# Performance work log

Hardware: AMD Instinct MI355X
Metric: run time of the kernel (lower is better)

Reference implementation:

```python
import jax, jax.numpy as jnp
import numpy as np

S_D, I_D, O_D = 256, 64, 64
BATCH, T = 64, 2048


def setup_inputs() -> dict:
    key = jax.random.key(0)
    ks = jax.random.split(key, 9)
    # state/inputs and raw standard-normal noise draws (torch.randn equivalents)
    state = jax.random.normal(ks[0], (BATCH, S_D), dtype=jnp.float32)
    inputs = jax.random.normal(ks[1], (BATCH, T, I_D), dtype=jnp.float32)
    eps_W = jax.random.normal(ks[2], (BATCH, T, S_D), dtype=jnp.float32)
    eps_V = jax.random.normal(ks[3], (BATCH, T, O_D), dtype=jnp.float32)
    # system matrices; F scaled to spectral radius ~0.95 (stable system)
    F = jax.random.normal(ks[4], (S_D, S_D), dtype=jnp.float32) * (0.95 / np.sqrt(S_D))
    B_mat = jax.random.normal(ks[5], (S_D, I_D), dtype=jnp.float32)
    H = jax.random.normal(ks[6], (O_D, S_D), dtype=jnp.float32)
    SNR = 2.0
    sqrt_S_W = jax.random.normal(ks[7], (S_D, S_D), dtype=jnp.float32) / SNR
    sqrt_S_V = jax.random.normal(ks[8], (O_D, O_D), dtype=jnp.float32) / SNR
    return {"state": state, "inputs": inputs, "eps_W": eps_W, "eps_V": eps_V,
            "F": F, "B_mat": B_mat, "H": H, "sqrt_S_W": sqrt_S_W, "sqrt_S_V": sqrt_S_V}


def reference(state, inputs, eps_W, eps_V, F, B_mat, H, sqrt_S_W, sqrt_S_V):
    # per-step drive: u_t = inputs_t @ B^T + W_t, with W_t = eps_W_t @ sqrt_S_W^T
    U = jnp.einsum('bti,si->bts', inputs, B_mat) + jnp.einsum('bts,ds->btd', eps_W, sqrt_S_W)
    V = jnp.einsum('bto,po->btp', eps_V, sqrt_S_V)  # [B, T, O_D]

    def step(s, u_t):  # s: [B, S_D], u_t: [B, S_D]
        s = s @ F.T + u_t
        return s, s

    _, states_t = jax.lax.scan(step, state, jnp.swapaxes(U, 0, 1))  # [T, B, S_D]
    states = jnp.swapaxes(states_t, 0, 1)  # [B, T, S_D]
    observations = jnp.einsum('bts,os->bto', states, H) + V  # [B, T, O_D]
    return states, observations
```

## Files before the change

kernel.cpp:

```cpp
#include <hip/hip_runtime.h>
#include <hip/hip_bf16.h>

#define S_DIM 256
#define I_DIM 64
#define O_DIM 64
#define BATCH 64
#define TT 2048
#define CHUNK 32
#define NCHUNK (TT / CHUNK)
#define NTASK (BATCH * TT / CHUNK)

typedef __attribute__((ext_vector_type(8))) short short8v;
typedef _Float16 half8v __attribute__((ext_vector_type(8)));
typedef __attribute__((ext_vector_type(4))) float float4v;

__device__ inline unsigned short f2bf(float f) {
  unsigned x = __float_as_uint(f);
  unsigned r = (x + 0x7FFFu + ((x >> 16) & 1u)) >> 16;
  return (unsigned short)r;
}
__device__ inline short bfr(float x) {
  __hip_bfloat16 h = __float2bfloat16(x);
  return __builtin_bit_cast(short, h);
}

__device__ inline void gload16(const float* g, float* lds) {
  __builtin_amdgcn_global_load_lds(
      (const __attribute__((address_space(1))) unsigned int*)g,
      (__attribute__((address_space(3))) unsigned int*)lds, 16, 0, 0);
}

__global__ void k_matsq(const float* __restrict__ src, float* __restrict__ dst) {
  const int i = blockIdx.x;
  const int j = threadIdx.x;
  float acc = 0.f;
#pragma unroll 8
  for (int k = 0; k < 256; ++k) acc += src[i * 256 + k] * src[k * 256 + j];
  dst[i * 256 + j] = acc;
}

__global__ void k_fsplit16(const float* __restrict__ src, _Float16* __restrict__ hi,
                           _Float16* __restrict__ lo) {
  int idx = blockIdx.x * 256 + threadIdx.x;
  float a = src[idx];
  _Float16 h = (_Float16)a;
  hi[idx] = h;
  lo[idx] = (_Float16)(a - (float)h);
}

__global__ void k_wcvt(const float* __restrict__ s1, const float* __restrict__ s2,
                       int K1, int K2, unsigned short* __restrict__ hi, int total) {
  int idx = blockIdx.x * 256 + threadIdx.x;
  if (idx >= total) return;
  int KT = K1 + K2;
  int n = idx / KT, k = idx - n * KT;
  float a = (k < K1) ? s1[n * K1 + k] : s2[n * K2 + (k - K1)];
  hi[idx] = f2bf(a);
}

template <int N_TOT, int K1, int K2, int M_TILE, int WIM, int WIN>
__global__ __launch_bounds__(256, 3) void k_tgemm(
    const float* __restrict__ A1, const float* __restrict__ A2,
    const unsigned short* __restrict__ W, float* __restrict__ out) {
  constexpr int KT = K1 + K2;
  constexpr int NKT = KT / 64;
  constexpr int MF = M_TILE / WIM / 16;
  constexpr int NF = N_TOT / WIN / 16;
  constexpr int LOGM = (M_TILE == 64) ? 6 : 7;
  constexpr int CPW = M_TILE / 16;

  __shared__ float als[2][M_TILE * 64];

  const int tid = threadIdx.x;
  const int wv = tid >> 6, lane = tid & 63;
  const int lo16 = lane & 15, hi4 = lane >> 4;
  const int wm = wv % WIM, wn = wv / WIM;
  const size_t R0 = (size_t)blockIdx.x * M_TILE;
  const int C0 = wn * (N_TOT / WIN);

  auto stage = [&](int buf, int kt) {
#pragma unroll
    for (int c = 0; c < CPW; ++c) {
      const int i = wv * CPW + c;
      const int s = i * 64 + lane;
      const int row = s & (M_TILE - 1);
      const int g = s >> LOGM;
      const int k0 = kt * 64;
      const float* src = (k0 < K1) ? A1 + (R0 + row) * K1 + k0 + g * 4
                                   : A2 + (R0 + row) * K2 + (k0 - K1) + g * 4;
      gload16(src, &als[buf][i * 256]);
    }
  };
  auto aread = [&](int buf, int kkl, int m, int h) -> float4 {
    const int row = wm * (M_TILE / WIM) + m * 16 + lo16;
    const int g = kkl * 8 + hi4 * 2 + h;
    return *reinterpret_cast<const float4*>(&als[buf][(g * M_TILE + row) * 4]);
  };
  auto wload = [&](int kk, int nf) -> short8v {
    return *reinterpret_cast<const short8v*>(
        W + (size_t)(C0 + nf * 16 + lo16) * KT + kk * 32 + hi4 * 8);
  };

  float4v acc[MF][NF];
#pragma unroll
  for (int m = 0; m < MF; ++m)
#pragma unroll
    for (int n = 0; n < NF; ++n) acc[m][n] = (float4v){0.f, 0.f, 0.f, 0.f};

  short8v wr[2][NF];
  stage(0, 0);
#pragma unroll
  for (int nf = 0; nf < NF; ++nf) wr[0][nf] = wload(0, nf);
  __syncthreads();

#pragma unroll
  for (int kt = 0; kt < NKT; ++kt) {
    if (kt + 1 < NKT) stage((kt + 1) & 1, kt + 1);
#pragma unroll
    for (int kkl = 0; kkl < 2; ++kkl) {
      const int kk = kt * 2 + kkl;
      if (kk + 1 < 2 * NKT) {
#pragma unroll
        for (int nf = 0; nf < NF; ++nf) wr[(kk + 1) & 1][nf] = wload(kk + 1, nf);
      }
      short8v ah[MF];
#pragma unroll
      for (int m = 0; m < MF; ++m) {
        float4 f0 = aread(kt & 1, kkl, m, 0);
        float4 f1 = aread(kt & 1, kkl, m, 1);
#pragma unroll
        for (int j = 0; j < 4; ++j) {
          ah[m][j] = bfr((&f0.x)[j]);
          ah[m][j + 4] = bfr((&f1.x)[j]);
        }
      }
#pragma unroll
      for (int nf = 0; nf < NF; ++nf)
#pragma unroll
        for (int m = 0; m < MF; ++m)
          acc[m][nf] = __builtin_amdgcn_mfma_f32_16x16x32_bf16(
              ah[m], wr[kk & 1][nf], acc[m][nf], 0, 0, 0);
    }
    __syncthreads();
  }

#pragma unroll
  for (int m = 0; m < MF; ++m)
#pragma unroll
    for (int nf = 0; nf < NF; ++nf) {
      const size_t r_base = R0 + wm * (M_TILE / WIM) + m * 16 + hi4 * 4;
      const int col = C0 + nf * 16 + lo16;
#pragma unroll
      for (int rr = 0; rr < 4; ++rr)
        out[(r_base + rr) * N_TOT + col] = acc[m][nf][rr];
    }
}

template <int MODE>
__global__ __launch_bounds__(1024, 4) void k_mscan(const _Float16* __restrict__ Fhi,
                                                   const _Float16* __restrict__ Flo,
                                                   float* __restrict__ U,
                                                   const float* __restrict__ E,
                                                   float* __restrict__ Lst) {
  __shared__ _Float16 sh[16 * 264];
  __shared__ _Float16 sl[16 * 264];

  const int tid = threadIdx.x;
  const int wv = tid >> 6;
  const int l = tid & 63;
  const int lo16 = l & 15, hi4 = l >> 4;
  const int dcol = wv * 16 + lo16;

  const int c = blockIdx.x >> 2;
  const int b0 = (blockIdx.x & 3) * 16;

  half8v fh[8], fl[8];
#pragma unroll
  for (int kk = 0; kk < 8; ++kk) {
    const size_t fo = (size_t)dcol * 256 + kk * 32 + hi4 * 8;
    fh[kk] = *reinterpret_cast<const half8v*>(Fhi + fo);
    fl[kk] = *reinterpret_cast<const half8v*>(Flo + fo);
  }

  if (MODE == 1) {
#pragma unroll
    for (int r = 0; r < 4; ++r) {
      const int m = hi4 * 4 + r;
      float x = E[((size_t)c * BATCH + b0 + m) * 256 + dcol];
      _Float16 h = (_Float16)x;
      sh[m * 264 + dcol] = h;
      sl[m * 264 + dcol] = (_Float16)(x - (float)h);
    }
    __syncthreads();
  }

  const size_t ustr = (size_t)TT * 256;
  float* ub = U + ((size_t)b0 * TT + c * CHUNK) * 256 + dcol;

  float u_cur[4], u_nxt[4];
#pragma unroll
  for (int r = 0; r < 4; ++r) u_cur[r] = ub[(size_t)(hi4 * 4 + r) * ustr];

  for (int k = 0; k < CHUNK; ++k) {
    if (k < CHUNK - 1) {
#pragma unroll
      for (int r = 0; r < 4; ++r)
        u_nxt[r] = ub[(size_t)(hi4 * 4 + r) * ustr + (k + 1) * 256];
    }
    float4v a0, a1, a2;
#pragma unroll
    for (int r = 0; r < 4; ++r) {
      a0[r] = u_cur[r];
      a1[r] = 0.f;
      a2[r] = 0.f;
    }

    if (MODE == 1 || k) {
#pragma unroll
      for (int kk = 0; kk < 8; ++kk) {
        const int ao = lo16 * 264 + kk * 32 + hi4 * 8;
        half8v ah = *reinterpret_cast<const half8v*>(&sh[ao]);
        half8v al = *reinterpret_cast<const half8v*>(&sl[ao]);
        a0 = __builtin_amdgcn_mfma_f32_16x16x32_f16(ah, fh[kk], a0, 0, 0, 0);
        a1 = __builtin_amdgcn_mfma_f32_16x16x32_f16(ah, fl[kk], a1, 0, 0, 0);
        a2 = __builtin_amdgcn_mfma_f32_16x16x32_f16(al, fh[kk], a2, 0, 0, 0);
      }
    }

    _Float16 xh[4], xl[4];
#pragma unroll
    for (int r = 0; r < 4; ++r) {
      float x = a0[r] + a1[r] + a2[r];
      if (MODE == 1) ub[(size_t)(hi4 * 4 + r) * ustr + k * 256] = x;
      if (MODE == 0 && k == CHUNK - 1)
        Lst[((size_t)c * BATCH + b0 + hi4 * 4 + r) * 256 + dcol] = x;
      _Float16 h = (_Float16)x;
      xh[r] = h;
      xl[r] = (_Float16)(x - (float)h);
    }
    __syncthreads();
#pragma unroll
    for (int r = 0; r < 4; ++r) {
      const int m = hi4 * 4 + r;
      sh[m * 264 + dcol] = xh[r];
      sl[m * 264 + dcol] = xl[r];
    }
    __syncthreads();
#pragma unroll
    for (int r = 0; r < 4; ++r) u_cur[r] = u_nxt[r];
  }
}

__global__ __launch_bounds__(1024, 4) void k_mcarry(const _Float16* __restrict__ FLhi,
                                                    const _Float16* __restrict__ FLlo,
                                                    const float* __restrict__ state0,
                                                    const float* __restrict__ Lst,
                                                    float* __restrict__ E) {
  __shared__ _Float16 sh[16 * 264];
  __shared__ _Float16 sl[16 * 264];

  const int tid = threadIdx.x;
  const int wv = tid >> 6;
  const int l = tid & 63;
  const int lo16 = l & 15, hi4 = l >> 4;
  const int dcol = wv * 16 + lo16;
  const int b0 = blockIdx.x * 16;

  half8v fh[8], fl[8];
#pragma unroll
  for (int kk = 0; kk < 8; ++kk) {
    const size_t fo = (size_t)dcol * 256 + kk * 32 + hi4 * 8;
    fh[kk] = *reinterpret_cast<const half8v*>(FLhi + fo);
    fl[kk] = *reinterpret_cast<const half8v*>(FLlo + fo);
  }

#pragma unroll
  for (int r = 0; r < 4; ++r) {
    const int m = hi4 * 4 + r;
    float x = state0[(size_t)(b0 + m) * 256 + dcol];
    E[(size_t)(b0 + m) * 256 + dcol] = x;
    _Float16 h = (_Float16)x;
    sh[m * 264 + dcol] = h;
    sl[m * 264 + dcol] = (_Float16)(x - (float)h);
  }
  __syncthreads();

  for (int cstep = 0; cstep < NCHUNK - 1; ++cstep) {
    float4v a0, a1, a2;
#pragma unroll
    for (int r = 0; r < 4; ++r) {
      a0[r] = Lst[((size_t)cstep * BATCH + b0 + hi4 * 4 + r) * 256 + dcol];
      a1[r] = 0.f;
      a2[r] = 0.f;
    }
#pragma unroll
    for (int kk = 0; kk < 8; ++kk) {
      const int ao = lo16 * 264 + kk * 32 + hi4 * 8;
      half8v ah = *reinterpret_cast<const half8v*>(&sh[ao]);
      half8v al = *reinterpret_cast<const half8v*>(&sl[ao]);
      a0 = __builtin_amdgcn_mfma_f32_16x16x32_f16(ah, fh[kk], a0, 0, 0, 0);
      a1 = __builtin_amdgcn_mfma_f32_16x16x32_f16(ah, fl[kk], a1, 0, 0, 0);
      a2 = __builtin_amdgcn_mfma_f32_16x16x32_f16(al, fh[kk], a2, 0, 0, 0);
    }
    _Float16 xh[4], xl[4];
#pragma unroll
    for (int r = 0; r < 4; ++r) {
      float x = a0[r] + a1[r] + a2[r];
      E[((size_t)(cstep + 1) * BATCH + b0 + hi4 * 4 + r) * 256 + dcol] = x;
      _Float16 h = (_Float16)x;
      xh[r] = h;
      xl[r] = (_Float16)(x - (float)h);
    }
    __syncthreads();
#pragma unroll
    for (int r = 0; r < 4; ++r) {
      const int m = hi4 * 4 + r;
      sh[m * 264 + dcol] = xh[r];
      sl[m * 264 + dcol] = xl[r];
    }
    __syncthreads();
  }
}

extern "C" void kernel_launch(void* const* d_in, const int* in_sizes, int n_in,
                              void* d_out, int out_size, void* d_ws, size_t ws_size,
                              hipStream_t stream) {
  const float* state  = (const float*)d_in[0];
  const float* inputs = (const float*)d_in[1];
  const float* eps_W  = (const float*)d_in[2];
  const float* eps_V  = (const float*)d_in[3];
  const float* F      = (const float*)d_in[4];
  const float* B_mat  = (const float*)d_in[5];
  const float* H      = (const float*)d_in[6];
  const float* SW     = (const float*)d_in[7];
  const float* SV     = (const float*)d_in[8];

  float* out = (float*)d_out;
  float* states_out = out;
  float* obs_out = out + (size_t)BATCH * TT * S_DIM;

  unsigned short* ws16 = (unsigned short*)d_ws;
  unsigned short* whi1 = ws16;
  unsigned short* whi2 = whi1 + 81920;
  _Float16* Fhi  = (_Float16*)(whi2 + 20480);
  _Float16* Flo  = Fhi + 65536;
  _Float16* FLhi = Flo + 65536;
  _Float16* FLlo = FLhi + 65536;

  float* Lst = obs_out;
  float* E   = Lst + (size_t)NCHUNK * BATCH * 256;
  float* Pa  = E + (size_t)NCHUNK * BATCH * 256;
  float* Pb  = Pa + 65536;

  k_matsq<<<256, 256, 0, stream>>>(F, Pa);
  k_matsq<<<256, 256, 0, stream>>>(Pa, Pb);
  k_matsq<<<256, 256, 0, stream>>>(Pb, Pa);
  k_matsq<<<256, 256, 0, stream>>>(Pa, Pb);
  k_matsq<<<256, 256, 0, stream>>>(Pb, Pa);

  k_fsplit16<<<256, 256, 0, stream>>>(F, Fhi, Flo);
  k_fsplit16<<<256, 256, 0, stream>>>(Pa, FLhi, FLlo);

  k_wcvt<<<320, 256, 0, stream>>>(B_mat, SW, 64, 256, whi1, 256 * 320);
  k_wcvt<<<80, 256, 0, stream>>>(H, SV, 256, 64, whi2, 64 * 320);

  k_tgemm<256, 64, 256, 64, 1, 4><<<BATCH * TT / 64, 256, 0, stream>>>(
      inputs, eps_W, whi1, states_out);

  k_mscan<0><<<NTASK / 16, 1024, 0, stream>>>(Fhi, Flo, states_out, E, Lst);

  k_mcarry<<<BATCH / 16, 1024, 0, stream>>>(FLhi, FLlo, state, Lst, E);

  k_mscan<1><<<NTASK / 16, 1024, 0, stream>>>(Fhi, Flo, states_out, E, Lst);

  k_tgemm<64, 256, 64, 128, 4, 1><<<BATCH * TT / 128, 256, 0, stream>>>(
      states_out, eps_V, whi2, obs_out);
}
```

Baseline: 425.0 us.

## Stage full 64x320 activation tile in LDS at once for GEMM kernels

Replaces the double-buffered K-tile streaming GEMM with a kernel that loads the whole 64-row by 320-wide fp32 activation tile into 80 KB of dynamic shared memory up front, then runs all MFMA steps with a single barrier. Weights are loaded directly per step instead of being register double-buffered. The output GEMM also switches from 128-row to 64-row tiles. This removes per-K-tile barriers and staging overlap, but the large LDS footprint limits occupancy to about one block per CU, so global-load latency is no longer hidden behind compute.

```diff
diff --git a/kernel.cpp b/kernel.cpp
--- a/kernel.cpp
+++ b/kernel.cpp
@@ -58,48 +58,39 @@
   hi[idx] = f2bf(a);
 }
 
-template <int N_TOT, int K1, int K2, int M_TILE, int WIM, int WIN>
-__global__ __launch_bounds__(256, 3) void k_tgemm(
-    const float* __restrict__ A1, const float* __restrict__ A2,
+template <int N_TOT, bool SMALL_FIRST, int WIM, int WIN>
+__global__ __launch_bounds__(256) void k_sgemm(
+    const float* __restrict__ Abig, const float* __restrict__ Asmall,
     const unsigned short* __restrict__ W, float* __restrict__ out) {
-  constexpr int KT = K1 + K2;
-  constexpr int NKT = KT / 64;
-  constexpr int MF = M_TILE / WIM / 16;
+  constexpr int KT = 320;
+  constexpr int MF = 64 / WIM / 16;
   constexpr int NF = N_TOT / WIN / 16;
-  constexpr int LOGM = (M_TILE == 64) ? 6 : 7;
-  constexpr int CPW = M_TILE / 16;
-
-  __shared__ float als[2][M_TILE * 64];
+  extern __shared__ float ls[];
 
   const int tid = threadIdx.x;
   const int wv = tid >> 6, lane = tid & 63;
   const int lo16 = lane & 15, hi4 = lane >> 4;
   const int wm = wv % WIM, wn = wv / WIM;
-  const size_t R0 = (size_t)blockIdx.x * M_TILE;
+  const size_t R0 = (size_t)blockIdx.x * 64;
   const int C0 = wn * (N_TOT / WIN);
 
-  auto stage = [&](int buf, int kt) {
-#pragma unroll
-    for (int c = 0; c < CPW; ++c) {
-      const int i = wv * CPW + c;
+#pragma unroll
+  for (int kt = 0; kt < 4; ++kt)
+#pragma unroll
+    for (int c = 0; c < 4; ++c) {
+      const int i = wv * 4 + c;
       const int s = i * 64 + lane;
-      const int row = s & (M_TILE - 1);
-      const int g = s >> LOGM;
-      const int k0 = kt * 64;
-      const float* src = (k0 < K1) ? A1 + (R0 + row) * K1 + k0 + g * 4
-                                   : A2 + (R0 + row) * K2 + (k0 - K1) + g * 4;
-      gload16(src, &als[buf][i * 256]);
-    }
-  };
-  auto aread = [&](int buf, int kkl, int m, int h) -> float4 {
-    const int row = wm * (M_TILE / WIM) + m * 16 + lo16;
-    const int g = kkl * 8 + hi4 * 2 + h;
-    return *reinterpret_cast<const float4*>(&als[buf][(g * M_TILE + row) * 4]);
-  };
-  auto wload = [&](int kk, int nf) -> short8v {
-    return *reinterpret_cast<const short8v*>(
-        W + (size_t)(C0 + nf * 16 + lo16) * KT + kk * 32 + hi4 * 8);
-  };
+      const int row = s & 63, g = s >> 6;
+      gload16(Abig + (R0 + row) * 256 + kt * 64 + g * 4, &ls[kt * 4096 + i * 256]);
+    }
+#pragma unroll
+  for (int c = 0; c < 4; ++c) {
+    const int i = wv * 4 + c;
+    const int s = i * 64 + lane;
+    const int row = s & 63, g = s >> 6;
+    gload16(Asmall + (R0 + row) * 64 + g * 4, &ls[16384 + i * 256]);
+  }
+  __syncthreads();
 
   float4v acc[MF][NF];
 #pragma unroll
@@ -107,48 +98,40 @@
 #pragma unroll
     for (int n = 0; n < NF; ++n) acc[m][n] = (float4v){0.f, 0.f, 0.f, 0.f};
 
-  short8v wr[2][NF];
-  stage(0, 0);
-#pragma unroll
-  for (int nf = 0; nf < NF; ++nf) wr[0][nf] = wload(0, nf);
-  __syncthreads();
-
-#pragma unroll
-  for (int kt = 0; kt < NKT; ++kt) {
-    if (kt + 1 < NKT) stage((kt + 1) & 1, kt + 1);
-#pragma unroll
-    for (int kkl = 0; kkl < 2; ++kkl) {
-      const int kk = kt * 2 + kkl;
-      if (kk + 1 < 2 * NKT) {
-#pragma unroll
-        for (int nf = 0; nf < NF; ++nf) wr[(kk + 1) & 1][nf] = wload(kk + 1, nf);
+#pragma unroll
+  for (int kw = 0; kw < 10; ++kw) {
+    const bool is_small = SMALL_FIRST ? (kw < 2) : (kw >= 8);
+    const int kl = SMALL_FIRST ? (is_small ? kw : kw - 2) : (is_small ? kw - 8 : kw);
+    short8v ah[MF];
+#pragma unroll
+    for (int m = 0; m < MF; ++m) {
+      const int row = wm * (64 / WIM) + m * 16 + lo16;
+      const float* base =
+          is_small ? &ls[16384 + ((kl * 8 + hi4 * 2) * 64 + row) * 4]
+                   : &ls[(kl >> 1) * 4096 + (((kl & 1) * 8 + hi4 * 2) * 64 + row) * 4];
+      float4 f0 = *reinterpret_cast<const float4*>(base);
+      float4 f1 = *reinterpret_cast<const float4*>(base + 256);
+#pragma unroll
+      for (int j = 0; j < 4; ++j) {
+        ah[m][j] = bfr((&f0.x)[j]);
+        ah[m][j + 4] = bfr((&f1.x)[j]);
       }
-      short8v ah[MF];
-#pragma unroll
-      for (int m = 0; m < MF; ++m) {
-        float4 f0 = aread(kt & 1, kkl, m, 0);
-        float4 f1 = aread(kt & 1, kkl, m, 1);
-#pragma unroll
-        for (int j = 0; j < 4; ++j) {
-          ah[m][j] = bfr((&f0.x)[j]);
-          ah[m][j + 4] = bfr((&f1.x)[j]);
-        }
-      }
-#pragma unroll
-      for (int nf = 0; nf < NF; ++nf)
-#pragma unroll
-        for (int m = 0; m < MF; ++m)
-          acc[m][nf] = __builtin_amdgcn_mfma_f32_16x16x32_bf16(
-              ah[m], wr[kk & 1][nf], acc[m][nf], 0, 0, 0);
-    }
-    __syncthreads();
+    }
+#pragma unroll
+    for (int nf = 0; nf < NF; ++nf) {
+      short8v w8 = *reinterpret_cast<const short8v*>(
+          W + (size_t)(C0 + nf * 16 + lo16) * KT + kw * 32 + hi4 * 8);
+#pragma unroll
+      for (int m = 0; m < MF; ++m)
+        acc[m][nf] = __builtin_amdgcn_mfma_f32_16x16x32_bf16(ah[m], w8, acc[m][nf], 0, 0, 0);
+    }
   }
 
 #pragma unroll
   for (int m = 0; m < MF; ++m)
 #pragma unroll
     for (int nf = 0; nf < NF; ++nf) {
-      const size_t r_base = R0 + wm * (M_TILE / WIM) + m * 16 + hi4 * 4;
+      const size_t r_base = R0 + wm * (64 / WIM) + m * 16 + hi4 * 4;
       const int col = C0 + nf * 16 + lo16;
 #pragma unroll
       for (int rr = 0; rr < 4; ++rr)
@@ -364,8 +347,8 @@
   k_wcvt<<<320, 256, 0, stream>>>(B_mat, SW, 64, 256, whi1, 256 * 320);
   k_wcvt<<<80, 256, 0, stream>>>(H, SV, 256, 64, whi2, 64 * 320);
 
-  k_tgemm<256, 64, 256, 64, 1, 4><<<BATCH * TT / 64, 256, 0, stream>>>(
-      inputs, eps_W, whi1, states_out);
+  k_sgemm<256, true, 1, 4><<<BATCH * TT / 64, 256, 81920, stream>>>(
+      eps_W, inputs, whi1, states_out);
 
   k_mscan<0><<<NTASK / 16, 1024, 0, stream>>>(Fhi, Flo, states_out, E, Lst);
 
@@ -373,6 +356,6 @@
 
   k_mscan<1><<<NTASK / 16, 1024, 0, stream>>>(Fhi, Flo, states_out, E, Lst);
 
-  k_tgemm<64, 256, 64, 128, 4, 1><<<BATCH * TT / 128, 256, 0, stream>>>(
+  k_sgemm<64, false, 4, 1><<<BATCH * TT / 64, 256, 81920, stream>>>(
       states_out, eps_V, whi2, obs_out);
 }
```

Measured after the change: 443.2 us. 1.04x slower.
